# Kernel optimization log

Hardware: AMD Instinct MI355X
Metric: run time of the kernel (lower is better)

## Reference

```python
import jax, jax.numpy as jnp
import numpy as np

TEMPERATURE = 0.2
EPS = 1e-10

def setup_inputs() -> dict:
    key = jax.random.key(0)
    x = jax.random.normal(key, (8, 1024, 64, 64), dtype=jnp.float32)
    return {"x": x}

def reference(x):
    B, C, H, W = x.shape
    xf = x.reshape(B, C, H * W)                      # [B, C, HW]
    dot = jnp.einsum('bcn,bdn->bcd', xf, xf) / TEMPERATURE  # [B, C, C]
    logits = jax.nn.softmax(dot, axis=-1)
    diag = jnp.diagonal(logits, axis1=-2, axis2=-1)  # [B, C]
    loss = -jnp.log(diag + EPS)
    return jnp.mean(loss)
```

## Files before the change

### kernel.cpp

```cpp
#include <hip/hip_runtime.h>
#include <hip/hip_bf16.h>

#define BATCH 8
#define CCH 1024
#define NHW 4096
#define SCALE 5.0f
#define ROWS (BATCH * CCH)

typedef unsigned char u8;
typedef unsigned int u32;
typedef __attribute__((ext_vector_type(4))) float float4v;
typedef __attribute__((ext_vector_type(4))) u32 uint4v;

__device__ __forceinline__ void async_load16(const void* gsrc, void* ldst) {
    __builtin_amdgcn_global_load_lds(
        (__attribute__((address_space(1))) void*)gsrc,
        (__attribute__((address_space(3))) void*)ldst,
        16, 0, 0);
}

__device__ __forceinline__ u32 pk4_fp8(float a, float b, float c, float d) {
    u32 v = __builtin_amdgcn_cvt_pk_fp8_f32(a, b, 0, false);
    v = __builtin_amdgcn_cvt_pk_fp8_f32(c, d, v, true);
    return v;
}

__device__ __forceinline__ float ssq4_fp8(u32 q) {
    float d0 = __builtin_amdgcn_cvt_f32_fp8(q, 0);
    float d1 = __builtin_amdgcn_cvt_f32_fp8(q, 1);
    float d2 = __builtin_amdgcn_cvt_f32_fp8(q, 2);
    float d3 = __builtin_amdgcn_cvt_f32_fp8(q, 3);
    return d0 * d0 + d1 * d1 + d2 * d2 + d3 * d3;
}

template <bool CONVERT>
__global__ __launch_bounds__(256) void prep_kernel(const float* __restrict__ x,
                                                   u8* __restrict__ xq,
                                                   float* __restrict__ diag,
                                                   float* __restrict__ l_acc) {
    const int row = blockIdx.x;
    const int tid = threadIdx.x;
    const float* src = x + (size_t)row * NHW;
    float ssum = 0.f;
#pragma unroll
    for (int p = 0; p < 4; ++p) {
        const int idx = p * 1024 + tid * 4;
        float4 v = *(const float4*)(src + idx);
        const u32 q = pk4_fp8(v.x, v.y, v.z, v.w);
        ssum += ssq4_fp8(q);
        if (CONVERT) *(u32*)(xq + (size_t)row * NHW + idx) = q;
    }
#pragma unroll
    for (int m = 1; m < 64; m <<= 1) ssum += __shfl_xor(ssum, m);
    __shared__ float red[4];
    if ((tid & 63) == 0) red[tid >> 6] = ssum;
    __syncthreads();
    if (tid == 0) {
        diag[row] = (red[0] + red[1] + red[2] + red[3]) * SCALE;
        l_acc[row] = 0.f;
    }
}

template <bool QSRC>
__global__ __launch_bounds__(256) void gram_kernel(const u8* __restrict__ Xq,
                                                   const float* __restrict__ Xf,
                                                   const float* __restrict__ diag,
                                                   float* __restrict__ l_acc,
                                                   float* __restrict__ num) {
    __shared__ __align__(16) u8 As[2][16384];
    __shared__ __align__(16) u8 Bs[2][8192];

    const int bid = blockIdx.x;
    const int b = bid & 7;
    const int t = bid >> 3;

    int bi = 0;
#pragma unroll
    for (int i = 7; i >= 1; --i) {
        if (t >= i * (17 - i)) { bi = i; break; }
    }
    const int bj2 = 2 * bi + (t - bi * (17 - bi));
    const bool aliasB = (bj2 == 2 * bi) || (bj2 == 2 * bi + 1);

    const int tid  = threadIdx.x;
    const int lane = tid & 63;
    const int w    = tid >> 6;
    const int wm   = w >> 1;
    const int wn   = w & 1;

    const int st_r  = lane >> 3;
    const int st_kc = (lane & 7) ^ st_r;

    const u8*    pA  = nullptr; const u8*    pB  = nullptr;
    const float* pAf = nullptr; const float* pBf = nullptr;
    if (QSRC) {
        const u8* baseX = Xq + (size_t)b * CCH * NHW;
        pA = baseX + (size_t)(bi * 128 + w * 32 + st_r) * NHW + st_kc * 16;
        pB = baseX + (size_t)(bj2 * 64 + w * 16 + st_r) * NHW + st_kc * 16;
    } else {
        const float* baseXf = Xf + (size_t)b * CCH * NHW;
        pAf = baseXf + (size_t)(bi * 128 + w * 32 + st_r) * NHW + st_kc * 16;
        pBf = baseXf + (size_t)(bj2 * 64 + w * 16 + st_r) * NHW + st_kc * 16;
    }

    float4v acc[4][2] = {};

    auto stage = [&](int buf, int K0) {
        if (QSRC) {
#pragma unroll
            for (int t8 = 0; t8 < 4; ++t8)
                async_load16(pA + (size_t)(t8 * 8) * NHW + K0,
                             As[buf] + (size_t)(w * 32 + t8 * 8) * 128);
            if (!aliasB) {
#pragma unroll
                for (int t8 = 0; t8 < 2; ++t8)
                    async_load16(pB + (size_t)(t8 * 8) * NHW + K0,
                                 Bs[buf] + (size_t)(w * 16 + t8 * 8) * 128);
            }
        } else {
#pragma unroll
            for (int t8 = 0; t8 < 4; ++t8) {
                const float* s = pAf + (size_t)(t8 * 8) * NHW + K0;
                float4 f0 = *(const float4*)(s);
                float4 f1 = *(const float4*)(s + 4);
                float4 f2 = *(const float4*)(s + 8);
                float4 f3 = *(const float4*)(s + 12);
                uint4v d;
                d.x = pk4_fp8(f0.x, f0.y, f0.z, f0.w);
                d.y = pk4_fp8(f1.x, f1.y, f1.z, f1.w);
                d.z = pk4_fp8(f2.x, f2.y, f2.z, f2.w);
                d.w = pk4_fp8(f3.x, f3.y, f3.z, f3.w);
                *(uint4v*)(As[buf] + (size_t)(w * 32 + t8 * 8 + st_r) * 128 + (lane & 7) * 16) = d;
            }
            if (!aliasB) {
#pragma unroll
                for (int t8 = 0; t8 < 2; ++t8) {
                    const float* s = pBf + (size_t)(t8 * 8) * NHW + K0;
                    float4 f0 = *(const float4*)(s);
                    float4 f1 = *(const float4*)(s + 4);
                    float4 f2 = *(const float4*)(s + 8);
                    float4 f3 = *(const float4*)(s + 12);
                    uint4v d;
                    d.x = pk4_fp8(f0.x, f0.y, f0.z, f0.w);
                    d.y = pk4_fp8(f1.x, f1.y, f1.z, f1.w);
                    d.z = pk4_fp8(f2.x, f2.y, f2.z, f2.w);
                    d.w = pk4_fp8(f3.x, f3.y, f3.z, f3.w);
                    *(uint4v*)(Bs[buf] + (size_t)(w * 16 + t8 * 8 + st_r) * 128 + (lane & 7) * 16) = d;
                }
            }
        }
    };

    stage(0, 0);
    __syncthreads();

    for (int i = 0; i < NHW / 128; ++i) {
        const int cur = i & 1;
        const int K0n = (i + 1) * 128;
        if (K0n < NHW) stage(cur ^ 1, K0n);

        const u8* Ab = As[cur];
        const u8* Bb = aliasB ? (Ab + (size_t)(bj2 - 2 * bi) * 64 * 128) : Bs[cur];
        const int q  = lane >> 4;
        const int rl = lane & 15;
#pragma unroll
        for (int s = 0; s < 4; ++s) {
            const int cbase = 2 * s + (q >> 1);
            const int boff  = (int)((cbase ^ (rl & 7)) * 16 + (q & 1) * 8);
            long af[4], bf[2];
#pragma unroll
            for (int mt = 0; mt < 4; ++mt)
                af[mt] = *(const long*)(Ab + (size_t)(wm * 64 + mt * 16 + rl) * 128 + boff);
#pragma unroll
            for (int nt = 0; nt < 2; ++nt)
                bf[nt] = *(const long*)(Bb + (size_t)(wn * 32 + nt * 16 + rl) * 128 + boff);
#pragma unroll
            for (int mt = 0; mt < 4; ++mt)
#pragma unroll
                for (int nt = 0; nt < 2; ++nt)
                    acc[mt][nt] = __builtin_amdgcn_mfma_f32_16x16x32_fp8_fp8(af[mt], bf[nt], acc[mt][nt], 0, 0, 0);
        }
        __syncthreads();
    }

    const int q  = lane >> 4;
    const int cl = lane & 15;
    const int rowbase = bi * 128 + wm * 64;
    const int colbase = bj2 * 64 + wn * 32;
    const float* dgb = diag + b * CCH;
    float* lb = l_acc + b * CCH;

#pragma unroll
    for (int mt = 0; mt < 4; ++mt) {
#pragma unroll
        for (int reg = 0; reg < 4; ++reg) {
            const int gr = rowbase + mt * 16 + q * 4 + reg;
            const float dg = dgb[gr];
            float s = 0.f;
#pragma unroll
            for (int nt = 0; nt < 2; ++nt) {
                const int gc = colbase + nt * 16 + cl;
                const float e = __expf(acc[mt][nt][reg] * SCALE - dg);
                if (gr <= gc) s += e;
                if (gr == gc) num[b * CCH + gr] = e;
            }
            s += __shfl_xor(s, 1);
            s += __shfl_xor(s, 2);
            s += __shfl_xor(s, 4);
            s += __shfl_xor(s, 8);
            if (cl == 0) atomicAdd(lb + gr, s);
        }
    }

#pragma unroll
    for (int nt = 0; nt < 2; ++nt) {
        const int gc = colbase + nt * 16 + cl;
        const float dgc = dgb[gc];
        float s = 0.f;
#pragma unroll
        for (int mt = 0; mt < 4; ++mt) {
#pragma unroll
            for (int reg = 0; reg < 4; ++reg) {
                const int gr = rowbase + mt * 16 + q * 4 + reg;
                if (gr < gc) s += __expf(acc[mt][nt][reg] * SCALE - dgc);
            }
        }
        s += __shfl_xor(s, 16);
        s += __shfl_xor(s, 32);
        if (lane < 16) atomicAdd(lb + gc, s);
    }
}

__global__ __launch_bounds__(1024) void finalize_kernel(const float* __restrict__ l_acc,
                                                        const float* __restrict__ num,
                                                        float* __restrict__ out) {
    const int tid = threadIdx.x;
    float s = 0.f;
    for (int r = tid; r < ROWS; r += 1024) {
        const float d = num[r] / l_acc[r];
        s += -__logf(d + 1e-10f);
    }
#pragma unroll
    for (int m = 1; m < 64; m <<= 1) s += __shfl_xor(s, m);
    __shared__ float red[16];
    if ((tid & 63) == 0) red[tid >> 6] = s;
    __syncthreads();
    if (tid == 0) {
        float tot = 0.f;
#pragma unroll
        for (int i = 0; i < 16; ++i) tot += red[i];
        out[0] = tot * (1.0f / (float)ROWS);
    }
}

extern "C" void kernel_launch(void* const* d_in, const int* in_sizes, int n_in,
                              void* d_out, int out_size, void* d_ws, size_t ws_size,
                              hipStream_t stream) {
    const float* x = (const float*)d_in[0];
    float* out = (float*)d_out;

    const size_t xq_bytes   = (size_t)BATCH * CCH * NHW;
    const size_t stat_bytes = (size_t)ROWS * 4;
    const bool fast = ws_size >= xq_bytes + 3 * stat_bytes;

    const int ntiles = 72;

    if (fast) {
        u8*    xq    = (u8*)d_ws;
        float* diag  = (float*)((char*)d_ws + xq_bytes);
        float* l_acc = diag + ROWS;
        float* num   = l_acc + ROWS;
        prep_kernel<true><<<ROWS, 256, 0, stream>>>(x, xq, diag, l_acc);
        gram_kernel<true><<<BATCH * ntiles, 256, 0, stream>>>(xq, nullptr, diag, l_acc, num);
        finalize_kernel<<<1, 1024, 0, stream>>>(l_acc, num, out);
    } else {
        float* diag  = (float*)d_ws;
        float* l_acc = diag + ROWS;
        float* num   = l_acc + ROWS;
        prep_kernel<false><<<ROWS, 256, 0, stream>>>(x, nullptr, diag, l_acc);
        gram_kernel<false><<<BATCH * ntiles, 256, 0, stream>>>(nullptr, x, diag, l_acc, num);
        finalize_kernel<<<1, 1024, 0, stream>>>(l_acc, num, out);
    }
}
```

Baseline: 240.9 us.

## Use 16x16x128 scaled FP8 MFMA and fuse finalize via last-block counter

The inner Gram loop now loads 32-byte fragments per row and issues one gfx950 scaled MFMA (16x16x128 f8f6f4, unit scales) per tile per K-slice, replacing four 16x16x32 FP8 MFMAs. This cuts MFMA instruction count and LDS load instructions. Separately, the finalize kernel is removed. The last gram block to finish, detected with an atomic counter and thread fences, computes the mean log loss, which saves one kernel launch. The risks are the fragment layout differing from what the new instruction expects, and extra fence and atomic overhead in every block.

```diff
diff --git a/kernel.cpp b/kernel.cpp
--- a/kernel.cpp
+++ b/kernel.cpp
@@ -11,6 +11,8 @@
 typedef unsigned int u32;
 typedef __attribute__((ext_vector_type(4))) float float4v;
 typedef __attribute__((ext_vector_type(4))) u32 uint4v;
+typedef __attribute__((ext_vector_type(4))) int i32x4;
+typedef __attribute__((ext_vector_type(8))) int i32x8;
 
 __device__ __forceinline__ void async_load16(const void* gsrc, void* ldst) {
     __builtin_amdgcn_global_load_lds(
@@ -37,7 +39,8 @@
 __global__ __launch_bounds__(256) void prep_kernel(const float* __restrict__ x,
                                                    u8* __restrict__ xq,
                                                    float* __restrict__ diag,
-                                                   float* __restrict__ l_acc) {
+                                                   float* __restrict__ l_acc,
+                                                   u32* __restrict__ counter) {
     const int row = blockIdx.x;
     const int tid = threadIdx.x;
     const float* src = x + (size_t)row * NHW;
@@ -58,6 +61,7 @@
     if (tid == 0) {
         diag[row] = (red[0] + red[1] + red[2] + red[3]) * SCALE;
         l_acc[row] = 0.f;
+        if (row == 0) *counter = 0;
     }
 }
 
@@ -66,7 +70,9 @@
                                                    const float* __restrict__ Xf,
                                                    const float* __restrict__ diag,
                                                    float* __restrict__ l_acc,
-                                                   float* __restrict__ num) {
+                                                   float* __restrict__ num,
+                                                   u32* __restrict__ counter,
+                                                   float* __restrict__ out) {
     __shared__ __align__(16) u8 As[2][16384];
     __shared__ __align__(16) u8 Bs[2][8192];
 
@@ -154,6 +160,11 @@
     stage(0, 0);
     __syncthreads();
 
+    const int q   = lane >> 4;
+    const int rl  = lane & 15;
+    const int rl7 = rl & 7;
+    const int c0  = 2 * q;
+
     for (int i = 0; i < NHW / 128; ++i) {
         const int cur = i & 1;
         const int K0n = (i + 1) * 128;
@@ -161,29 +172,33 @@
 
         const u8* Ab = As[cur];
         const u8* Bb = aliasB ? (Ab + (size_t)(bj2 - 2 * bi) * 64 * 128) : Bs[cur];
-        const int q  = lane >> 4;
-        const int rl = lane & 15;
-#pragma unroll
-        for (int s = 0; s < 4; ++s) {
-            const int cbase = 2 * s + (q >> 1);
-            const int boff  = (int)((cbase ^ (rl & 7)) * 16 + (q & 1) * 8);
-            long af[4], bf[2];
-#pragma unroll
-            for (int mt = 0; mt < 4; ++mt)
-                af[mt] = *(const long*)(Ab + (size_t)(wm * 64 + mt * 16 + rl) * 128 + boff);
+
+        i32x8 af[4], bf[2];
+#pragma unroll
+        for (int mt = 0; mt < 4; ++mt) {
+            const u8* p = Ab + (size_t)(wm * 64 + mt * 16 + rl) * 128;
+            i32x4 lo = *(const i32x4*)(p + ((c0    ) ^ rl7) * 16);
+            i32x4 hi = *(const i32x4*)(p + ((c0 + 1) ^ rl7) * 16);
+            af[mt] = __builtin_shufflevector(lo, hi, 0, 1, 2, 3, 4, 5, 6, 7);
+        }
+#pragma unroll
+        for (int nt = 0; nt < 2; ++nt) {
+            const u8* p = Bb + (size_t)(wn * 32 + nt * 16 + rl) * 128;
+            i32x4 lo = *(const i32x4*)(p + ((c0    ) ^ rl7) * 16);
+            i32x4 hi = *(const i32x4*)(p + ((c0 + 1) ^ rl7) * 16);
+            bf[nt] = __builtin_shufflevector(lo, hi, 0, 1, 2, 3, 4, 5, 6, 7);
+        }
+#pragma unroll
+        for (int mt = 0; mt < 4; ++mt)
 #pragma unroll
             for (int nt = 0; nt < 2; ++nt)
-                bf[nt] = *(const long*)(Bb + (size_t)(wn * 32 + nt * 16 + rl) * 128 + boff);
-#pragma unroll
-            for (int mt = 0; mt < 4; ++mt)
-#pragma unroll
-                for (int nt = 0; nt < 2; ++nt)
-                    acc[mt][nt] = __builtin_amdgcn_mfma_f32_16x16x32_fp8_fp8(af[mt], bf[nt], acc[mt][nt], 0, 0, 0);
-        }
+                acc[mt][nt] = __builtin_amdgcn_mfma_scale_f32_16x16x128_f8f6f4(
+                    af[mt], bf[nt], acc[mt][nt],
+                    0 , 0 ,
+                    0, 127 , 0, 127 );
         __syncthreads();
     }
 
-    const int q  = lane >> 4;
     const int cl = lane & 15;
     const int rowbase = bi * 128 + wm * 64;
     const int colbase = bj2 * 64 + wn * 32;
@@ -229,27 +244,29 @@
         s += __shfl_xor(s, 32);
         if (lane < 16) atomicAdd(lb + gc, s);
     }
-}
-
-__global__ __launch_bounds__(1024) void finalize_kernel(const float* __restrict__ l_acc,
-                                                        const float* __restrict__ num,
-                                                        float* __restrict__ out) {
-    const int tid = threadIdx.x;
-    float s = 0.f;
-    for (int r = tid; r < ROWS; r += 1024) {
-        const float d = num[r] / l_acc[r];
-        s += -__logf(d + 1e-10f);
-    }
-#pragma unroll
-    for (int m = 1; m < 64; m <<= 1) s += __shfl_xor(s, m);
-    __shared__ float red[16];
-    if ((tid & 63) == 0) red[tid >> 6] = s;
+
+    __shared__ u32 lastflag;
+    __threadfence();
     __syncthreads();
     if (tid == 0) {
-        float tot = 0.f;
-#pragma unroll
-        for (int i = 0; i < 16; ++i) tot += red[i];
-        out[0] = tot * (1.0f / (float)ROWS);
+        const u32 old = atomicAdd(counter, 1);
+        lastflag = (old == (u32)(gridDim.x - 1)) ? 1u : 0u;
+    }
+    __syncthreads();
+    if (lastflag) {
+        __threadfence();
+        float s = 0.f;
+        for (int r = tid; r < ROWS; r += 256) {
+            const float d = num[r] / l_acc[r];
+            s += -__logf(d + 1e-10f);
+        }
+#pragma unroll
+        for (int m = 1; m < 64; m <<= 1) s += __shfl_xor(s, m);
+        __shared__ float red[4];
+        if ((tid & 63) == 0) red[tid >> 6] = s;
+        __syncthreads();
+        if (tid == 0)
+            out[0] = (red[0] + red[1] + red[2] + red[3]) * (1.0f / (float)ROWS);
     }
 }
 
@@ -261,24 +278,24 @@
 
     const size_t xq_bytes   = (size_t)BATCH * CCH * NHW;
     const size_t stat_bytes = (size_t)ROWS * 4;
-    const bool fast = ws_size >= xq_bytes + 3 * stat_bytes;
+    const bool fast = ws_size >= xq_bytes + 3 * stat_bytes + 64;
 
     const int ntiles = 72;
 
     if (fast) {
-        u8*    xq    = (u8*)d_ws;
-        float* diag  = (float*)((char*)d_ws + xq_bytes);
-        float* l_acc = diag + ROWS;
-        float* num   = l_acc + ROWS;
-        prep_kernel<true><<<ROWS, 256, 0, stream>>>(x, xq, diag, l_acc);
-        gram_kernel<true><<<BATCH * ntiles, 256, 0, stream>>>(xq, nullptr, diag, l_acc, num);
-        finalize_kernel<<<1, 1024, 0, stream>>>(l_acc, num, out);
+        u8*    xq      = (u8*)d_ws;
+        float* diag    = (float*)((char*)d_ws + xq_bytes);
+        float* l_acc   = diag + ROWS;
+        float* num     = l_acc + ROWS;
+        u32*   counter = (u32*)(num + ROWS);
+        prep_kernel<true><<<ROWS, 256, 0, stream>>>(x, xq, diag, l_acc, counter);
+        gram_kernel<true><<<BATCH * ntiles, 256, 0, stream>>>(xq, nullptr, diag, l_acc, num, counter, out);
     } else {
-        float* diag  = (float*)d_ws;
-        float* l_acc = diag + ROWS;
-        float* num   = l_acc + ROWS;
-        prep_kernel<false><<<ROWS, 256, 0, stream>>>(x, nullptr, diag, l_acc);
-        gram_kernel<false><<<BATCH * ntiles, 256, 0, stream>>>(nullptr, x, diag, l_acc, num);
-        finalize_kernel<<<1, 1024, 0, stream>>>(l_acc, num, out);
-    }
-}
+        float* diag    = (float*)d_ws;
+        float* l_acc   = diag + ROWS;
+        float* num     = l_acc + ROWS;
+        u32*   counter = (u32*)(num + ROWS);
+        prep_kernel<false><<<ROWS, 256, 0, stream>>>(x, nullptr, diag, l_acc, counter);
+        gram_kernel<false><<<BATCH * ntiles, 256, 0, stream>>>(nullptr, x, diag, l_acc, num, counter, out);
+    }
+}
```

New measurement: 302.7 us. 1.26x slower.
